# Kernel tuning notes

Hardware: AMD Instinct MI355X
Metric: run time of the kernel (lower is better)

The kernel has to match this reference:

```python
import jax, jax.numpy as jnp
import numpy as np

DIM = 64

def conv2d_g2(x, w, b):
    # 3x3 conv, padding=1, groups=2, NCHW
    y = jax.lax.conv_general_dilated(x, w, (1, 1), [(1, 1), (1, 1)],
                                     dimension_numbers=('NCHW', 'OIHW', 'NCHW'),
                                     feature_group_count=2)
    return y + b[None, :, None, None]

def bilinear_gather(x, py, px):
    # x: [B,C,H,W]; py,px: [B,K,H,W] float sample coords -> [B,K,H,W,C]
    B, C, H, W = x.shape
    y0 = jnp.floor(py); x0 = jnp.floor(px)
    ly = py - y0; lx = px - x0
    hy = 1.0 - ly; hx = 1.0 - lx
    b_idx = jnp.arange(B)[:, None, None, None]
    def gather(yi, xi):
        valid = (yi >= 0) & (yi < H) & (xi >= 0) & (xi < W)
        yc = jnp.clip(yi, 0, H - 1).astype(jnp.int32)
        xc = jnp.clip(xi, 0, W - 1).astype(jnp.int32)
        v = x[b_idx, :, yc, xc]  # [B,K,H,W,C]
        return v * valid[..., None].astype(x.dtype)
    return (gather(y0, x0) * (hy * hx)[..., None]
            + gather(y0, x0 + 1) * (hy * lx)[..., None]
            + gather(y0 + 1, x0) * (ly * hx)[..., None]
            + gather(y0 + 1, x0 + 1) * (ly * lx)[..., None])

def deform_dw(x, offset, w, b, k, pad, dil):
    # depthwise (groups=C, offset_groups=1) deformable conv, stride 1
    B, C, H, W = x.shape
    K = k * k
    off = offset.reshape(B, K, 2, H, W)  # torchvision layout: (dy,dx) per kernel tap
    ky = jnp.repeat(jnp.arange(k), k).astype(x.dtype)   # [K]
    kx = jnp.tile(jnp.arange(k), k).astype(x.dtype)     # [K]
    base_y = jnp.arange(H, dtype=x.dtype)[None, None, :, None] - pad + dil * ky[None, :, None, None]
    base_x = jnp.arange(W, dtype=x.dtype)[None, None, None, :] - pad + dil * kx[None, :, None, None]
    py = base_y + off[:, :, 0]  # [B,K,H,W]
    px = base_x + off[:, :, 1]
    val = bilinear_gather(x, py, px)  # [B,K,H,W,C]
    return jnp.einsum('bkhwc,ck->bchw', val, w.reshape(C, K)) + b[None, :, None, None]

def lsk_forward(x, w_off3, b_off3, w_off2, b_off2, w7, b7, w5, b5):
    B, C, H, W = x.shape
    offset3 = conv2d_g2(x, w_off3, b_off3)            # [B,98,H,W]
    out1 = deform_dw(x, offset3, w7, b7, 7, 9, 3)     # [B,C,H,W]
    offset2 = conv2d_g2(x, w_off2, b_off2)            # [B,50,H,W]
    out2 = deform_dw(out1, offset2, w5, b5, 5, 6, 3)  # [B,C,H,W]
    feats = jnp.stack([out1, out2], axis=1)           # [B,2,C,H,W]
    gap = feats.mean(axis=(3, 4), keepdims=True)      # [B,2,C,1,1]
    attn = jax.nn.softmax(gap, axis=1)
    return jnp.sum(feats * attn, axis=1)              # [B,C,H,W]

def setup_inputs() -> dict:
    key = jax.random.key(0)
    ks = jax.random.split(key, 9)
    B, C, H, W = 4, DIM, 56, 56
    return {
        'x':      jax.random.normal(ks[0], (B, C, H, W), jnp.float32),
        'w_off3': jax.random.normal(ks[1], (98, C // 2, 3, 3), jnp.float32) * 0.05,
        'b_off3': jax.random.normal(ks[2], (98,), jnp.float32) * 0.05,
        'w_off2': jax.random.normal(ks[3], (50, C // 2, 3, 3), jnp.float32) * 0.05,
        'b_off2': jax.random.normal(ks[4], (50,), jnp.float32) * 0.05,
        'w7':     jax.random.normal(ks[5], (C, 1, 7, 7), jnp.float32) * 0.1,
        'b7':     jax.random.normal(ks[6], (C,), jnp.float32) * 0.05,
        'w5':     jax.random.normal(ks[7], (C, 1, 5, 5), jnp.float32) * 0.1,
        'b5':     jax.random.normal(ks[8], (C,), jnp.float32) * 0.05,
    }

def reference(x, w_off3, b_off3, w_off2, b_off2, w7, b7, w5, b5):
    return lsk_forward(x, w_off3, b_off3, w_off2, b_off2, w7, b7, w5, b5)
```

## Files before the change

kernel.cpp:

```cpp
#include <hip/hip_runtime.h>
#include <hip/hip_fp16.h>
#include <math.h>

#define HH 56
#define WW 56
#define CC 64
#define BB 4
#define HWA (HH*WW)

typedef _Float16 half8_t __attribute__((ext_vector_type(8)));
typedef _Float16 h2_t   __attribute__((ext_vector_type(2)));
typedef float f32x4_t __attribute__((ext_vector_type(4)));

__global__ __launch_bounds__(256)
void k_prep(const float* __restrict__ x,
            const float* __restrict__ w3, const float* __restrict__ w2,
            const float* __restrict__ b3, const float* __restrict__ b2,
            __half2* __restrict__ xp, _Float16* __restrict__ xh,
            _Float16* __restrict__ Wp, float* __restrict__ bbp) {
    int blk = blockIdx.x;
    int tid = threadIdx.x;
    if (blk < BB*56) {
        __shared__ float ld[64*57];
        int b = blk / 56, y = blk % 56;
        for (int i = tid; i < 64*56; i += 256) {
            int c = i / 56, col = i % 56;
            ld[c*57 + col] = x[((size_t)b*CC + c)*HWA + y*WW + col];
        }
        __syncthreads();
        for (int i = tid; i < 57*64; i += 256) {
            int j = i >> 6, c = i & 63;
            float lo = (j > 0)  ? ld[c*57 + j - 1] : 0.f;
            float hi = (j < 56) ? ld[c*57 + j]     : 0.f;
            xp[((size_t)(b*HH + y)*57 + j)*CC + c] = __floats2half2_rn(lo, hi);
        }
        _Float16* dst = xh + (((size_t)(b*2)*56 + y)*58)*32;
        for (int i = tid; i < 2*58*32; i += 256) {
            int g = i / 1856;
            int r = i % 1856;
            int col = r / 32, ic = r % 32;
            float v = 0.f;
            if (col >= 1 && col <= 56) v = ld[(g*32 + ic)*57 + col - 1];
            dst[(size_t)g*56*58*32 + r] = (_Float16)v;
        }
    } else {
        int i = (blk - BB*56)*256 + tid;
        if (i < 46080) {
            int j    = i & 7;
            int lane = (i >> 3) & 63;
            int mt   = (i >> 9) % 5;
            int kt   = (i / 2560) % 9;
            int g    = i / 23040;
            int m  = mt*16 + (lane & 15);
            int ic = (lane >> 4)*8 + j;
            int ky = kt/3, kx = kt%3;
            float v = 0.f;
            if (m < 49)      v = w3[((g*49 + m)*32 + ic)*9 + ky*3 + kx];
            else if (m < 74) v = w2[((g*25 + (m-49))*32 + ic)*9 + ky*3 + kx];
            Wp[i] = (_Float16)v;
        } else if (i < 46080 + 160) {
            int t = i - 46080; int g = t/80, m = t%80;
            float v = 0.f;
            if (m < 49)      v = b3[g*49 + m];
            else if (m < 74) v = b2[g*25 + (m-49)];
            bbp[t] = v;
        }
    }
}

__global__ void k_pairo(const float* __restrict__ o, __half2* __restrict__ xp) {
    __shared__ float ld[56*64];
    int blk = blockIdx.x;
    int b = blk / 56, y = blk % 56;
    int tid = threadIdx.x;
    for (int i = tid; i < 56*64; i += 256)
        ld[i] = o[((size_t)b*HWA + y*WW)*CC + i];
    __syncthreads();
    for (int i = tid; i < 57*64; i += 256) {
        int j = i >> 6, c = i & 63;
        float lo = (j > 0)  ? ld[(j-1)*64 + c] : 0.f;
        float hi = (j < 56) ? ld[j*64 + c]     : 0.f;
        xp[((size_t)(b*HH + y)*57 + j)*CC + c] = __floats2half2_rn(lo, hi);
    }
}

__global__ __launch_bounds__(64)
void k_convmfma(const _Float16* __restrict__ xh, const _Float16* __restrict__ Wp,
                const float* __restrict__ bb,
                float* __restrict__ off3, float* __restrict__ off2) {
    __shared__ _Float16 tile[3*18*32];
    int blk = blockIdx.x;
    int nq = blk & 3;
    int t  = blk >> 2;
    int iy = t % 56;
    int g  = (t / 56) & 1;
    int b  = t / 112;
    int lane = threadIdx.x;
    int n0 = nq * 16;

    const unsigned int* xs = (const unsigned int*)xh;
    unsigned int* tl = (unsigned int*)tile;
#pragma unroll
    for (int i = 0; i < 14; ++i) {
        int idx = i*64 + lane;
        if (idx < 864) {
            int ic2 = idx & 15;
            int seg = idx >> 4;
            int cl = seg % 18, r = seg / 18;
            int y = iy - 1 + r, col = n0 + cl;
            unsigned int v = 0;
            if (y >= 0 && y < 56 && col < 58)
                v = xs[(((size_t)(b*2+g)*56 + y)*58 + col)*16 + ic2];
            tl[idx] = v;
        }
    }
    __syncthreads();

    int nlo = lane & 15, khi = lane >> 4;
    f32x4_t acc[5];
#pragma unroll
    for (int mt = 0; mt < 5; ++mt) acc[mt] = (f32x4_t){0.f,0.f,0.f,0.f};

    const half8_t* wp8 = (const half8_t*)Wp;
#pragma unroll
    for (int kt = 0; kt < 9; ++kt) {
        int ky = kt/3, kx = kt%3;
        half8_t bfrag = *(const half8_t*)&tile[((ky*18) + nlo + kx)*32 + khi*8];
#pragma unroll
        for (int mt = 0; mt < 5; ++mt) {
            half8_t afrag = wp8[(((size_t)g*9 + kt)*5 + mt)*64 + lane];
            acc[mt] = __builtin_amdgcn_mfma_f32_16x16x32_f16(afrag, bfrag, acc[mt], 0, 0, 0);
        }
    }

    int pixcol = n0 + nlo;
    if (pixcol < 56) {
        int pix = iy*WW + pixcol;
#pragma unroll
        for (int mt = 0; mt < 5; ++mt) {
#pragma unroll
            for (int r = 0; r < 4; ++r) {
                int m = mt*16 + khi*4 + r;
                if (m < 74) {
                    float val = acc[mt][r] + bb[g*80 + m];
                    if (m < 49)
                        off3[((size_t)b*98 + g*49 + m)*HWA + pix] = val;
                    else
                        off2[((size_t)b*50 + g*25 + (m-49))*HWA + pix] = val;
                }
            }
        }
    }
}

template<int K, int KS, int PAD>
__global__ void k_deform(const h2_t* __restrict__ xp, const float* __restrict__ off,
                         const float* __restrict__ wg, const float* __restrict__ bias,
                         float* __restrict__ out, float* __restrict__ partial) {
    __shared__ float lw[K*65];
    __shared__ float loffs[2*K][4];
    __shared__ int4  lmeta[4][K];
    __shared__ float red[4][64];
    int tid = threadIdx.x + threadIdx.y*64;
    int blk = blockIdx.x;
    int xcd = blk & 7;
    int idx = blk >> 3;
    int b   = xcd >> 1;
    int hw0 = (xcd & 1)*(HWA/2) + idx*4;

    for (int i = tid; i < K*64; i += 256) {
        int c = i / K, t = i % K;
        lw[t*65 + c] = wg[i];
    }
    if (tid < 2*K) {
        float4 v = *(const float4*)&off[((size_t)b*2*K + tid)*HWA + hw0];
        loffs[tid][0] = v.x; loffs[tid][1] = v.y;
        loffs[tid][2] = v.z; loffs[tid][3] = v.w;
    }
    __syncthreads();
    if (tid < 4*K) {
        int p = tid / K, t = tid % K;
        int hw = hw0 + p;
        int h = hw / WW, w = hw % WW;
        int ky = t / KS, kx = t % KS;
        float py = (float)(h - PAD + 3*ky) + loffs[2*t][p];
        float px = (float)(w - PAD + 3*kx) + loffs[2*t+1][p];
        float y0f = floorf(py), x0f = floorf(px);
        float ly = py - y0f, lx = px - x0f;
        float hy = 1.f - ly, hx = 1.f - lx;
        int y0 = (int)y0f, x0 = (int)x0f;
        int j = x0 + 1;
        bool jv = (j >= 0) && (j <= 56);
        int jc = jv ? j : 0;
        float s0 = ((y0   >= 0) && (y0   < HH) && jv) ? hy : 0.f;
        float s1 = ((y0+1 >= 0) && (y0+1 < HH) && jv) ? ly : 0.f;
        int y0c = min(max(y0,   0), HH-1);
        int y1c = min(max(y0+1, 0), HH-1);
        int4 m;
        m.x = (y0c*57 + jc)*64;
        m.y = (y1c*57 + jc)*64;
        __half2 wa = __floats2half2_rn(s0*hx, s0*lx);
        __half2 wb = __floats2half2_rn(s1*hx, s1*lx);
        m.z = *(int*)&wa;
        m.w = *(int*)&wb;
        lmeta[p][t] = m;
    }
    __syncthreads();

    int yp = threadIdx.y;
    int c  = threadIdx.x;
    const h2_t* xb = xp + (size_t)b*HH*57*CC + c;

    float acc = 0.f;
#pragma unroll 2
    for (int t = 0; t < K; ++t) {
        int4 m = lmeta[yp][t];
        h2_t r0 = xb[m.x];
        h2_t r1 = xb[m.y];
        h2_t wA = *(h2_t*)&m.z;
        h2_t wB = *(h2_t*)&m.w;
        float v = __builtin_amdgcn_fdot2(r0, wA, 0.f, false);
        v = __builtin_amdgcn_fdot2(r1, wB, v, false);
        acc = fmaf(v, lw[t*65 + c], acc);
    }
    float val = acc + bias[c];
    out[((size_t)b*HWA + hw0 + yp)*CC + c] = val;
    red[yp][c] = val;
    __syncthreads();
    if (yp == 0)
        partial[((size_t)b*(HWA/4) + (hw0 >> 2))*64 + c]
            = red[0][c] + red[1][c] + red[2][c] + red[3][c];
}

__global__ void k_gapA(const float* __restrict__ p1, const float* __restrict__ p2,
                       float* __restrict__ g2) {
    __shared__ float red[4][64];
    int blk = blockIdx.x;
    int chunk = blk % 14;
    int bf    = blk / 14;
    int b     = bf >> 1;
    const float* p = (bf & 1) ? p2 : p1;
    int tid = threadIdx.x;
    int c = tid & 63, s = tid >> 6;
    float sum = 0.f;
#pragma unroll
    for (int i = 0; i < 14; ++i) {
        int j = chunk*56 + s + 4*i;
        sum += p[((size_t)b*(HWA/4) + j)*64 + c];
    }
    red[s][c] = sum;
    __syncthreads();
    if (s == 0)
        g2[((size_t)bf*14 + chunk)*64 + c]
            = red[0][c] + red[1][c] + red[2][c] + red[3][c];
}

__global__ void k_combine(const float* __restrict__ o1, const float* __restrict__ o2,
                          const float* __restrict__ g2, float* __restrict__ out) {
    __shared__ float tile[64][65];
    __shared__ float gsh[2][64];
    int blk = blockIdx.x;
    int b   = blk / (HWA/64);
    int t0  = (blk % (HWA/64)) * 64;
    int tid = threadIdx.x;
    int c = tid & 63, q = tid >> 6;

    if (tid < 128) {
        int f = tid >> 6, cc = tid & 63;
        float s = 0.f;
#pragma unroll
        for (int k = 0; k < 14; ++k)
            s += g2[((size_t)(b*2+f)*14 + k)*64 + cc];
        gsh[f][cc] = s * (1.f/HWA);
    }
    __syncthreads();

    float g1v = gsh[0][c];
    float g2v = gsh[1][c];
    float m  = fmaxf(g1v, g2v);
    float e1 = expf(g1v - m), e2 = expf(g2v - m);
    float a1 = e1 / (e1 + e2), a2 = 1.f - a1;

#pragma unroll
    for (int i = 0; i < 16; ++i) {
        int p = q + 4*i;
        size_t idx = ((size_t)b*HWA + t0 + p)*CC + c;
        tile[p][c] = o1[idx]*a1 + o2[idx]*a2;
    }
    __syncthreads();
    int p2 = tid & 63;
#pragma unroll
    for (int i = 0; i < 16; ++i) {
        int c2 = q + 4*i;
        out[((size_t)b*CC + c2)*HWA + t0 + p2] = tile[p2][c2];
    }
}

extern "C" void kernel_launch(void* const* d_in, const int* in_sizes, int n_in,
                              void* d_out, int out_size, void* d_ws, size_t ws_size,
                              hipStream_t stream) {
    const float* x      = (const float*)d_in[0];
    const float* w_off3 = (const float*)d_in[1];
    const float* b_off3 = (const float*)d_in[2];
    const float* w_off2 = (const float*)d_in[3];
    const float* b_off2 = (const float*)d_in[4];
    const float* w7     = (const float*)d_in[5];
    const float* b7     = (const float*)d_in[6];
    const float* w5     = (const float*)d_in[7];
    const float* b5     = (const float*)d_in[8];
    float* out = (float*)d_out;

    float* ws    = (float*)d_ws;
    float* off3r = ws;
    float* off2r = off3r + 1229312;
    float* out1  = off2r + 627200;
    float* out2  = out1  + 802816;
    float* xp1f  = out2  + 802816;
    float* xhf   = xp1f  + 817152;
    float* part1 = xhf   + 415744;
    float* part2 = part1 + 200704;
    float* gpA   = part2 + 200704;
    float* wpf   = gpA   + 7168;
    float* bbp   = wpf   + 23040;
    __half2*  xp1 = (__half2*)xp1f;
    __half2*  xp2 = (__half2*)off3r;
    _Float16* xh  = (_Float16*)xhf;
    _Float16* Wp  = (_Float16*)wpf;
    size_t need = (size_t)(1229312 + 627200 + 802816*2 + 817152 + 415744
                           + 200704*2 + 7168 + 23040 + 160) * 4;
    if (ws_size < need) return;

    k_prep<<<BB*56 + 181, 256, 0, stream>>>(x, w_off3, w_off2, b_off3, b_off2,
                                            xp1, xh, Wp, bbp);
    k_convmfma<<<BB*2*56*4, 64, 0, stream>>>(xh, Wp, bbp, off3r, off2r);
    k_deform<49,7,9><<<BB*(HWA/4), dim3(64,4), 0, stream>>>(
        (const h2_t*)xp1, off3r, w7, b7, out1, part1);
    k_pairo<<<BB*56, 256, 0, stream>>>(out1, xp2);
    k_deform<25,5,6><<<BB*(HWA/4), dim3(64,4), 0, stream>>>(
        (const h2_t*)xp2, off2r, w5, b5, out2, part2);
    k_gapA<<<8*14, 256, 0, stream>>>(part1, part2, gpA);
    k_combine<<<BB*(HWA/64), 256, 0, stream>>>(out1, out2, gpA, out);
}
```

Before: 162.7 us.

## Fuse pair-packing into first deform kernel and merge conv blocks into 4-wave blocks

The first deformable conv kernel now writes its output directly into the half-precision horizontally paired layout the second deform kernel reads, which removes the separate k_pairo pass and its extra read of out1. The paired buffer moves to its own workspace region instead of aliasing off3. The offset conv kernel now puts the four column-quarter waves of a row in one 256-thread block with per-wave tiles instead of four 64-thread blocks. The fused writes are scattered 2-byte stores, and the workspace grows.

```diff
diff --git a/kernel.cpp b/kernel.cpp
--- a/kernel.cpp
+++ b/kernel.cpp
@@ -68,38 +68,21 @@
     }
 }
 
-__global__ void k_pairo(const float* __restrict__ o, __half2* __restrict__ xp) {
-    __shared__ float ld[56*64];
-    int blk = blockIdx.x;
-    int b = blk / 56, y = blk % 56;
-    int tid = threadIdx.x;
-    for (int i = tid; i < 56*64; i += 256)
-        ld[i] = o[((size_t)b*HWA + y*WW)*CC + i];
-    __syncthreads();
-    for (int i = tid; i < 57*64; i += 256) {
-        int j = i >> 6, c = i & 63;
-        float lo = (j > 0)  ? ld[(j-1)*64 + c] : 0.f;
-        float hi = (j < 56) ? ld[j*64 + c]     : 0.f;
-        xp[((size_t)(b*HH + y)*57 + j)*CC + c] = __floats2half2_rn(lo, hi);
-    }
-}
-
-__global__ __launch_bounds__(64)
+__global__ __launch_bounds__(256)
 void k_convmfma(const _Float16* __restrict__ xh, const _Float16* __restrict__ Wp,
                 const float* __restrict__ bb,
                 float* __restrict__ off3, float* __restrict__ off2) {
-    __shared__ _Float16 tile[3*18*32];
-    int blk = blockIdx.x;
-    int nq = blk & 3;
-    int t  = blk >> 2;
-    int iy = t % 56;
-    int g  = (t / 56) & 1;
-    int b  = t / 112;
+    __shared__ _Float16 tile[4][3*18*32];
+    int blk = blockIdx.x;
+    int iy = blk % 56;
+    int g  = (blk / 56) & 1;
+    int b  = blk / 112;
+    int wv   = threadIdx.y;
     int lane = threadIdx.x;
-    int n0 = nq * 16;
+    int n0 = wv * 16;
 
     const unsigned int* xs = (const unsigned int*)xh;
-    unsigned int* tl = (unsigned int*)tile;
+    unsigned int* tl = (unsigned int*)&tile[wv][0];
 #pragma unroll
     for (int i = 0; i < 14; ++i) {
         int idx = i*64 + lane;
@@ -125,7 +108,7 @@
 #pragma unroll
     for (int kt = 0; kt < 9; ++kt) {
         int ky = kt/3, kx = kt%3;
-        half8_t bfrag = *(const half8_t*)&tile[((ky*18) + nlo + kx)*32 + khi*8];
+        half8_t bfrag = *(const half8_t*)&tile[wv][((ky*18) + nlo + kx)*32 + khi*8];
 #pragma unroll
         for (int mt = 0; mt < 5; ++mt) {
             half8_t afrag = wp8[(((size_t)g*9 + kt)*5 + mt)*64 + lane];
@@ -153,10 +136,11 @@
     }
 }
 
-template<int K, int KS, int PAD>
+template<int K, int KS, int PAD, bool WP>
 __global__ void k_deform(const h2_t* __restrict__ xp, const float* __restrict__ off,
                          const float* __restrict__ wg, const float* __restrict__ bias,
-                         float* __restrict__ out, float* __restrict__ partial) {
+                         float* __restrict__ out, float* __restrict__ partial,
+                         _Float16* __restrict__ xpo) {
     __shared__ float lw[K*65];
     __shared__ float loffs[2*K][4];
     __shared__ int4  lmeta[4][K];
@@ -224,7 +208,19 @@
         acc = fmaf(v, lw[t*65 + c], acc);
     }
     float val = acc + bias[c];
-    out[((size_t)b*HWA + hw0 + yp)*CC + c] = val;
+    int hw = hw0 + yp;
+    out[((size_t)b*HWA + hw)*CC + c] = val;
+
+    if (WP) {
+        int y = hw / WW, w = hw % WW;
+        _Float16* base = xpo + ((size_t)(b*HH + y)*57)*CC*2;
+        _Float16 hv = (_Float16)val;
+        base[((w    )*64 + c)*2 + 1] = hv;
+        base[((w + 1)*64 + c)*2 + 0] = hv;
+        if (w == 0)  base[(c)*2 + 0] = (_Float16)0.f;
+        if (w == 55) base[((56)*64 + c)*2 + 1] = (_Float16)0.f;
+    }
+
     red[yp][c] = val;
     __syncthreads();
     if (yp == 0)
@@ -316,28 +312,28 @@
     float* out1  = off2r + 627200;
     float* out2  = out1  + 802816;
     float* xp1f  = out2  + 802816;
-    float* xhf   = xp1f  + 817152;
+    float* xp2f  = xp1f  + 817152;
+    float* xhf   = xp2f  + 817152;
     float* part1 = xhf   + 415744;
     float* part2 = part1 + 200704;
     float* gpA   = part2 + 200704;
     float* wpf   = gpA   + 7168;
     float* bbp   = wpf   + 23040;
     __half2*  xp1 = (__half2*)xp1f;
-    __half2*  xp2 = (__half2*)off3r;
+    _Float16* xp2h = (_Float16*)xp2f;
     _Float16* xh  = (_Float16*)xhf;
     _Float16* Wp  = (_Float16*)wpf;
-    size_t need = (size_t)(1229312 + 627200 + 802816*2 + 817152 + 415744
+    size_t need = (size_t)(1229312 + 627200 + 802816*2 + 817152*2 + 415744
                            + 200704*2 + 7168 + 23040 + 160) * 4;
     if (ws_size < need) return;
 
     k_prep<<<BB*56 + 181, 256, 0, stream>>>(x, w_off3, w_off2, b_off3, b_off2,
                                             xp1, xh, Wp, bbp);
-    k_convmfma<<<BB*2*56*4, 64, 0, stream>>>(xh, Wp, bbp, off3r, off2r);
-    k_deform<49,7,9><<<BB*(HWA/4), dim3(64,4), 0, stream>>>(
-        (const h2_t*)xp1, off3r, w7, b7, out1, part1);
-    k_pairo<<<BB*56, 256, 0, stream>>>(out1, xp2);
-    k_deform<25,5,6><<<BB*(HWA/4), dim3(64,4), 0, stream>>>(
-        (const h2_t*)xp2, off2r, w5, b5, out2, part2);
+    k_convmfma<<<BB*2*56, dim3(64,4), 0, stream>>>(xh, Wp, bbp, off3r, off2r);
+    k_deform<49,7,9,true><<<BB*(HWA/4), dim3(64,4), 0, stream>>>(
+        (const h2_t*)xp1, off3r, w7, b7, out1, part1, xp2h);
+    k_deform<25,5,6,false><<<BB*(HWA/4), dim3(64,4), 0, stream>>>(
+        (const h2_t*)xp2f, off2r, w5, b5, out2, part2, nullptr);
     k_gapA<<<8*14, 256, 0, stream>>>(part1, part2, gpA);
     k_combine<<<BB*(HWA/64), 256, 0, stream>>>(out1, out2, gpA, out);
 }
```

Measured after the change: 155.6 us. -4.4%, faster.
